# Kernel optimization log

Measured on AMD Instinct MI355X. Metric: run time of the kernel, lower is better.

## Reference

```python
import jax, jax.numpy as jnp
import numpy as np

ADJ_SIZE = 512
START_POS = 128
END_POS = 384
IN_FEATURES = 128
OUT_FEATURES = 128
BATCH = 64
BN_EPS = 1e-5


def setup_inputs() -> dict:
    key = jax.random.key(0)
    k1, k2, k3 = jax.random.split(key, 3)
    inputs = {
        "input": jax.random.normal(k1, (BATCH, ADJ_SIZE, IN_FEATURES), dtype=jnp.float32),
        "adj": jax.random.uniform(k2, (BATCH, ADJ_SIZE, ADJ_SIZE), dtype=jnp.float32),
        "weight": jax.random.normal(k3, (IN_FEATURES, OUT_FEATURES), dtype=jnp.float32) * (1.0 / np.sqrt(IN_FEATURES)),
        "gamma": jnp.ones((OUT_FEATURES * ADJ_SIZE,), dtype=jnp.float32),
        "beta": jnp.zeros((OUT_FEATURES * ADJ_SIZE,), dtype=jnp.float32),
    }
    return inputs


def _crop_mask(n, s, e, dtype):
    # zeros everywhere except the [s:e, s:e] crop block, set to 1
    idx = jnp.arange(n)
    in_crop = (idx >= s) & (idx < e)
    return (in_crop[:, None] & in_crop[None, :]).astype(dtype)  # [N, N]


def reference(input, adj, weight, gamma, beta):
    B, N, _ = input.shape
    # support = input @ weight : [B, N, F_out]
    support = jnp.einsum('bni,io->bno', input, weight)
    # mask adjacency to the crop block
    mask = _crop_mask(N, START_POS, END_POS, adj.dtype)
    adj_ = adj * mask  # [B, N, N]
    # aggregated output : [B, N, F_out]
    output_ = jnp.einsum('bnm,bmf->bnf', adj_, support)
    F = output_.shape[2]
    # BatchNorm1d over flattened (N * F) features, training-mode batch stats
    x = output_.reshape(B, N * F)
    mean = jnp.mean(x, axis=0)
    var = jnp.mean(jnp.square(x - mean), axis=0)  # biased variance (torch BN)
    x_hat = (x - mean) * jax.lax.rsqrt(var + BN_EPS)
    y = x_hat * gamma + beta
    return y.reshape(B, N, F)
```

## Files before the change

### kernel.cpp

```cpp
#include <hip/hip_runtime.h>
#include <hip/hip_bf16.h>

#define BATCH 64
#define NADJ  512
#define F     128
#define CROP0 128
#define CROP1 384
#define CN    256
#define BN_EPS 1e-5f

typedef __attribute__((ext_vector_type(8))) short short8;
typedef __attribute__((ext_vector_type(4))) float f32x4;

__device__ __forceinline__ ushort f2bf(float x) {
  __hip_bfloat16 h = __float2bfloat16(x);
  return *reinterpret_cast<ushort*>(&h);
}

__device__ __forceinline__ float bf2f(ushort u) {
  const unsigned v = (unsigned)u << 16;
  float f;
  __builtin_memcpy(&f, &v, 4);
  return f;
}

__device__ __forceinline__ short8 cvt8(const float4 a, const float4 b) {
  short8 r;
  r[0] = (short)f2bf(a.x); r[1] = (short)f2bf(a.y);
  r[2] = (short)f2bf(a.z); r[3] = (short)f2bf(a.w);
  r[4] = (short)f2bf(b.x); r[5] = (short)f2bf(b.y);
  r[6] = (short)f2bf(b.z); r[7] = (short)f2bf(b.w);
  return r;
}

__global__ __launch_bounds__(512, 1) void gcn_ka(
    const float* __restrict__ input, const float* __restrict__ adj,
    const float* __restrict__ W, const float* __restrict__ beta,
    float* __restrict__ out, ushort* __restrict__ Ocrop) {
  const int x = blockIdx.x & 7, y = blockIdx.x >> 3;
  const int b  = ((y >> 2) << 3) | x;
  const int qt = y & 3;
  __shared__ ushort wt[128][136];
  __shared__ ushort ain[2][64][136];
  __shared__ ushort stl[128][268];
  const int tid = threadIdx.x;
  const int l = tid & 63, w = tid >> 6;
  const int lr = l & 15, lg = l >> 4;

  const int n0  = qt * 64 + (w & 3) * 16;
  const int wf0 = (w >> 2) * 64;
  const float* a0 =
      adj + ((size_t)b * NADJ + CROP0 + n0 + lr) * NADJ + CROP0;
  float4 xreg[16];
#pragma unroll
  for (int ks = 0; ks < 8; ++ks) {
    const int k0 = ks * 32 + lg * 8;
    xreg[2 * ks]     = *reinterpret_cast<const float4*>(&a0[k0]);
    xreg[2 * ks + 1] = *reinterpret_cast<const float4*>(&a0[k0 + 4]);
  }

  {
    const int gid = blockIdx.x * 512 + tid;
#pragma unroll
    for (int q = 0; q < 4; ++q) {
      const int g2 = gid + q * 131072;
      const int c4 = (g2 & 31) * 4;
      const int rr = (g2 >> 5) & 255;
      const int bb = g2 >> 13;
      const int n  = rr < 128 ? rr : rr + 256;
      const float4 bv =
          *reinterpret_cast<const float4*>(&beta[(size_t)n * F + c4]);
      *reinterpret_cast<float4*>(&out[((size_t)bb * NADJ + n) * F + c4]) = bv;
    }
  }

  {
    const int i0 = tid & 63;
    const int fq = (tid >> 6) * 16;
#pragma unroll
    for (int ih = 0; ih < 2; ++ih) {
      const int i = i0 + ih * 64;
      const float* wr = &W[(size_t)i * F + fq];
      float4 v[4];
#pragma unroll
      for (int q = 0; q < 4; ++q)
        v[q] = reinterpret_cast<const float4*>(wr)[q];
#pragma unroll
      for (int q = 0; q < 4; ++q) {
        wt[fq + q * 4 + 0][i] = f2bf(v[q].x);
        wt[fq + q * 4 + 1][i] = f2bf(v[q].y);
        wt[fq + q * 4 + 2][i] = f2bf(v[q].z);
        wt[fq + q * 4 + 3][i] = f2bf(v[q].w);
      }
    }
  }

  const float* inb = input + ((size_t)b * NADJ + CROP0) * F;
  const int msub = (w & 3) * 16;
  const int sf0  = (w >> 2) * 64;
  const int ml0  = tid >> 5;
  const int ic4  = (tid & 31) * 4;
  float4 pv[4];
#pragma unroll
  for (int q = 0; q < 4; ++q)
    pv[q] = *reinterpret_cast<const float4*>(
        &inb[(size_t)(ml0 + q * 16) * F + ic4]);

  short8 areg[8];
#pragma unroll
  for (int ks = 0; ks < 8; ++ks)
    areg[ks] = cvt8(xreg[2 * ks], xreg[2 * ks + 1]);

#pragma unroll
  for (int q = 0; q < 4; ++q)
    *reinterpret_cast<ushort4*>(&ain[0][ml0 + q * 16][ic4]) =
        make_ushort4(f2bf(pv[q].x), f2bf(pv[q].y), f2bf(pv[q].z),
                     f2bf(pv[q].w));
  __syncthreads();

  f32x4 acc[4] = {};
#pragma unroll
  for (int cc = 0; cc < 4; ++cc) {
    const int mc = cc * 64;
    if (cc < 3) {
#pragma unroll
      for (int q = 0; q < 4; ++q)
        pv[q] = *reinterpret_cast<const float4*>(
            &inb[(size_t)(mc + 64 + ml0 + q * 16) * F + ic4]);
    }
    if (cc > 0) {
      const int kb0 = mc - 64;
#pragma unroll
      for (int ks2 = 0; ks2 < 2; ++ks2) {
        const int ks = (cc - 1) * 2 + ks2;
        const int k0 = kb0 + ks2 * 32 + lg * 8;
#pragma unroll
        for (int fi = 0; fi < 4; ++fi) {
          const short8 bv =
              *reinterpret_cast<const short8*>(&stl[wf0 + fi * 16 + lr][k0]);
          acc[fi] = __builtin_amdgcn_mfma_f32_16x16x32_bf16(areg[ks], bv,
                                                            acc[fi], 0, 0, 0);
        }
      }
    }
    f32x4 sacc[4] = {};
#pragma unroll
    for (int ks = 0; ks < 4; ++ks) {
      const int k0 = ks * 32 + lg * 8;
      const short8 av =
          *reinterpret_cast<const short8*>(&ain[cc & 1][msub + lr][k0]);
#pragma unroll
      for (int fi = 0; fi < 4; ++fi) {
        const short8 bv =
            *reinterpret_cast<const short8*>(&wt[sf0 + fi * 16 + lr][k0]);
        sacc[fi] =
            __builtin_amdgcn_mfma_f32_16x16x32_bf16(av, bv, sacc[fi], 0, 0, 0);
      }
    }
#pragma unroll
    for (int fi = 0; fi < 4; ++fi)
      *reinterpret_cast<ushort4*>(
          &stl[sf0 + fi * 16 + lr][mc + msub + lg * 4]) =
          make_ushort4(f2bf(sacc[fi][0]), f2bf(sacc[fi][1]),
                       f2bf(sacc[fi][2]), f2bf(sacc[fi][3]));
    if (cc < 3) {
#pragma unroll
      for (int q = 0; q < 4; ++q)
        *reinterpret_cast<ushort4*>(&ain[(cc + 1) & 1][ml0 + q * 16][ic4]) =
            make_ushort4(f2bf(pv[q].x), f2bf(pv[q].y), f2bf(pv[q].z),
                         f2bf(pv[q].w));
    }
    __syncthreads();
  }

#pragma unroll
  for (int ks2 = 0; ks2 < 2; ++ks2) {
    const int ks = 6 + ks2;
    const int k0 = 192 + ks2 * 32 + lg * 8;
#pragma unroll
    for (int fi = 0; fi < 4; ++fi) {
      const short8 bv =
          *reinterpret_cast<const short8*>(&stl[wf0 + fi * 16 + lr][k0]);
      acc[fi] = __builtin_amdgcn_mfma_f32_16x16x32_bf16(areg[ks], bv, acc[fi],
                                                        0, 0, 0);
    }
  }

#pragma unroll
  for (int fi = 0; fi < 4; ++fi) {
    const int f = wf0 + fi * 16 + lr;
    const int n = n0 + lg * 4;
#pragma unroll
    for (int r = 0; r < 4; ++r)
      Ocrop[((size_t)b * CN + n + r) * F + f] = f2bf(acc[fi][r]);
  }
}

__global__ __launch_bounds__(256) void gcn_kb(
    const ushort* __restrict__ Ocrop, float* __restrict__ out,
    const float* __restrict__ gamma, const float* __restrict__ beta) {
  __shared__ f32x4 s_l[256], s2_l[256];
  __shared__ f32x4 m_l[32], r_l[32];
  const int tid = threadIdx.x;
  const int qq = tid & 31, bg = tid >> 5;
  const int j  = (blockIdx.x * 32 + qq) * 4;
  const int nl = j >> 7, f = j & 127;
  const int nf = (CROP0 + nl) * F + f;
  const ushort* p = Ocrop + (size_t)j + (size_t)bg * 8 * CN * F;

  f32x4 x[8];
  f32x4 s = {0.f, 0.f, 0.f, 0.f}, s2 = {0.f, 0.f, 0.f, 0.f};
#pragma unroll
  for (int bb = 0; bb < 8; ++bb) {
    const ushort4 u =
        *reinterpret_cast<const ushort4*>(&p[(size_t)bb * CN * F]);
    f32x4 v;
    v[0] = bf2f(u.x); v[1] = bf2f(u.y); v[2] = bf2f(u.z); v[3] = bf2f(u.w);
    x[bb] = v;
    s += v;
    s2 += v * v;
  }
  s_l[tid]  = s;
  s2_l[tid] = s2;
  __syncthreads();
  if (tid < 32) {
    f32x4 ts = {0.f, 0.f, 0.f, 0.f}, ts2 = {0.f, 0.f, 0.f, 0.f};
#pragma unroll
    for (int g = 0; g < 8; ++g) {
      ts += s_l[g * 32 + tid];
      ts2 += s2_l[g * 32 + tid];
    }
    const f32x4 mean = ts * (1.f / BATCH);
    const f32x4 var  = ts2 * (1.f / BATCH) - mean * mean;
    f32x4 rs;
    rs[0] = rsqrtf(var[0] + BN_EPS);
    rs[1] = rsqrtf(var[1] + BN_EPS);
    rs[2] = rsqrtf(var[2] + BN_EPS);
    rs[3] = rsqrtf(var[3] + BN_EPS);
    m_l[tid] = mean;
    r_l[tid] = rs;
  }
  __syncthreads();
  const f32x4 mean = m_l[qq];
  const f32x4 rs   = r_l[qq];
  const float4 gm = *reinterpret_cast<const float4*>(&gamma[nf]);
  const float4 bt = *reinterpret_cast<const float4*>(&beta[nf]);
  f32x4 a, c;
  a[0] = rs[0] * gm.x; a[1] = rs[1] * gm.y;
  a[2] = rs[2] * gm.z; a[3] = rs[3] * gm.w;
  c[0] = bt.x - mean[0] * a[0]; c[1] = bt.y - mean[1] * a[1];
  c[2] = bt.z - mean[2] * a[2]; c[3] = bt.w - mean[3] * a[3];
#pragma unroll
  for (int bb = 0; bb < 8; ++bb) {
    const f32x4 y = x[bb] * a + c;
    *reinterpret_cast<f32x4*>(
        &out[(size_t)nf + (size_t)(bg * 8 + bb) * NADJ * F]) = y;
  }
}

extern "C" void kernel_launch(void* const* d_in, const int* in_sizes, int n_in,
                              void* d_out, int out_size, void* d_ws,
                              size_t ws_size, hipStream_t stream) {
  const float* input = (const float*)d_in[0];
  const float* adj   = (const float*)d_in[1];
  const float* W     = (const float*)d_in[2];
  const float* gamma = (const float*)d_in[3];
  const float* beta  = (const float*)d_in[4];
  float* out = (float*)d_out;

  ushort* Ocrop = (ushort*)d_ws;

  gcn_ka<<<256, 512, 0, stream>>>(input, adj, W, beta, out, Ocrop);
  gcn_kb<<<256, 256, 0, stream>>>(Ocrop, out, gamma, beta);
}
```

Measured before the change: 23.15 us.

## Reassociate GCN product as (adj·X)·W to avoid redundant support computation

Instead of each block recomputing the full support X·W for the crop and then multiplying by its adjacency rows, each block first computes adj_block·X and then multiplies that 64-row result by W. This removes the redundant per-block full-crop X·W and roughly halves the matrix-core work per block. The input is now loaded and transposed into LDS in one pass rather than double-buffered chunks, which removes overlap and adds scalar transposed LDS stores. The intermediate is rounded to bf16 at a different point, which changes numerics slightly.

```diff
diff --git a/kernel.cpp b/kernel.cpp
--- a/kernel.cpp
+++ b/kernel.cpp
@@ -40,17 +40,17 @@
   const int x = blockIdx.x & 7, y = blockIdx.x >> 3;
   const int b  = ((y >> 2) << 3) | x;
   const int qt = y & 3;
+  __shared__ ushort xt[128][280];
   __shared__ ushort wt[128][136];
-  __shared__ ushort ain[2][64][136];
-  __shared__ ushort stl[128][268];
+  __shared__ ushort tt[64][136];
   const int tid = threadIdx.x;
   const int l = tid & 63, w = tid >> 6;
   const int lr = l & 15, lg = l >> 4;
 
-  const int n0  = qt * 64 + (w & 3) * 16;
-  const int wf0 = (w >> 2) * 64;
+  const int n0w = qt * 64 + (w & 3) * 16;
+  const int wh  = w >> 2;
   const float* a0 =
-      adj + ((size_t)b * NADJ + CROP0 + n0 + lr) * NADJ + CROP0;
+      adj + ((size_t)b * NADJ + CROP0 + n0w + lr) * NADJ + CROP0;
   float4 xreg[16];
 #pragma unroll
   for (int ks = 0; ks < 8; ++ks) {
@@ -96,100 +96,69 @@
   }
 
   const float* inb = input + ((size_t)b * NADJ + CROP0) * F;
-  const int msub = (w & 3) * 16;
-  const int sf0  = (w >> 2) * 64;
-  const int ml0  = tid >> 5;
-  const int ic4  = (tid & 31) * 4;
-  float4 pv[4];
-#pragma unroll
-  for (int q = 0; q < 4; ++q)
-    pv[q] = *reinterpret_cast<const float4*>(
-        &inb[(size_t)(ml0 + q * 16) * F + ic4]);
+#pragma unroll
+  for (int q = 0; q < 16; ++q) {
+    const int idx = tid + q * 512;
+    const int m   = idx >> 5;
+    const int c4  = (idx & 31) * 4;
+    const float4 v =
+        *reinterpret_cast<const float4*>(&inb[(size_t)m * F + c4]);
+    xt[c4 + 0][m] = f2bf(v.x);
+    xt[c4 + 1][m] = f2bf(v.y);
+    xt[c4 + 2][m] = f2bf(v.z);
+    xt[c4 + 3][m] = f2bf(v.w);
+  }
 
   short8 areg[8];
 #pragma unroll
   for (int ks = 0; ks < 8; ++ks)
     areg[ks] = cvt8(xreg[2 * ks], xreg[2 * ks + 1]);
 
-#pragma unroll
-  for (int q = 0; q < 4; ++q)
-    *reinterpret_cast<ushort4*>(&ain[0][ml0 + q * 16][ic4]) =
-        make_ushort4(f2bf(pv[q].x), f2bf(pv[q].y), f2bf(pv[q].z),
-                     f2bf(pv[q].w));
-  __syncthreads();
-
-  f32x4 acc[4] = {};
-#pragma unroll
-  for (int cc = 0; cc < 4; ++cc) {
-    const int mc = cc * 64;
-    if (cc < 3) {
-#pragma unroll
-      for (int q = 0; q < 4; ++q)
-        pv[q] = *reinterpret_cast<const float4*>(
-            &inb[(size_t)(mc + 64 + ml0 + q * 16) * F + ic4]);
-    }
-    if (cc > 0) {
-      const int kb0 = mc - 64;
-#pragma unroll
-      for (int ks2 = 0; ks2 < 2; ++ks2) {
-        const int ks = (cc - 1) * 2 + ks2;
-        const int k0 = kb0 + ks2 * 32 + lg * 8;
-#pragma unroll
-        for (int fi = 0; fi < 4; ++fi) {
-          const short8 bv =
-              *reinterpret_cast<const short8*>(&stl[wf0 + fi * 16 + lr][k0]);
-          acc[fi] = __builtin_amdgcn_mfma_f32_16x16x32_bf16(areg[ks], bv,
-                                                            acc[fi], 0, 0, 0);
-        }
-      }
-    }
-    f32x4 sacc[4] = {};
-#pragma unroll
-    for (int ks = 0; ks < 4; ++ks) {
-      const int k0 = ks * 32 + lg * 8;
-      const short8 av =
-          *reinterpret_cast<const short8*>(&ain[cc & 1][msub + lr][k0]);
-#pragma unroll
-      for (int fi = 0; fi < 4; ++fi) {
-        const short8 bv =
-            *reinterpret_cast<const short8*>(&wt[sf0 + fi * 16 + lr][k0]);
-        sacc[fi] =
-            __builtin_amdgcn_mfma_f32_16x16x32_bf16(av, bv, sacc[fi], 0, 0, 0);
-      }
-    }
-#pragma unroll
-    for (int fi = 0; fi < 4; ++fi)
-      *reinterpret_cast<ushort4*>(
-          &stl[sf0 + fi * 16 + lr][mc + msub + lg * 4]) =
-          make_ushort4(f2bf(sacc[fi][0]), f2bf(sacc[fi][1]),
-                       f2bf(sacc[fi][2]), f2bf(sacc[fi][3]));
-    if (cc < 3) {
-#pragma unroll
-      for (int q = 0; q < 4; ++q)
-        *reinterpret_cast<ushort4*>(&ain[(cc + 1) & 1][ml0 + q * 16][ic4]) =
-            make_ushort4(f2bf(pv[q].x), f2bf(pv[q].y), f2bf(pv[q].z),
-                         f2bf(pv[q].w));
-    }
-    __syncthreads();
-  }
-
-#pragma unroll
-  for (int ks2 = 0; ks2 < 2; ++ks2) {
-    const int ks = 6 + ks2;
-    const int k0 = 192 + ks2 * 32 + lg * 8;
+  __syncthreads();
+
+  const int if0 = wh * 64;
+  f32x4 accT[4] = {};
+#pragma unroll
+  for (int ks = 0; ks < 8; ++ks) {
+    const int k0 = ks * 32 + lg * 8;
 #pragma unroll
     for (int fi = 0; fi < 4; ++fi) {
       const short8 bv =
-          *reinterpret_cast<const short8*>(&stl[wf0 + fi * 16 + lr][k0]);
-      acc[fi] = __builtin_amdgcn_mfma_f32_16x16x32_bf16(areg[ks], bv, acc[fi],
-                                                        0, 0, 0);
-    }
-  }
-
+          *reinterpret_cast<const short8*>(&xt[if0 + fi * 16 + lr][k0]);
+      accT[fi] = __builtin_amdgcn_mfma_f32_16x16x32_bf16(areg[ks], bv,
+                                                         accT[fi], 0, 0, 0);
+    }
+  }
+  const int nloc = (w & 3) * 16;
 #pragma unroll
   for (int fi = 0; fi < 4; ++fi) {
-    const int f = wf0 + fi * 16 + lr;
-    const int n = n0 + lg * 4;
+    const int i = if0 + fi * 16 + lr;
+#pragma unroll
+    for (int r = 0; r < 4; ++r)
+      tt[nloc + lg * 4 + r][i] = f2bf(accT[fi][r]);
+  }
+  __syncthreads();
+
+  const int f0 = wh * 64;
+  f32x4 acc[4] = {};
+#pragma unroll
+  for (int ks = 0; ks < 4; ++ks) {
+    const int k0 = ks * 32 + lg * 8;
+    const short8 av =
+        *reinterpret_cast<const short8*>(&tt[nloc + lr][k0]);
+#pragma unroll
+    for (int fi = 0; fi < 4; ++fi) {
+      const short8 bv =
+          *reinterpret_cast<const short8*>(&wt[f0 + fi * 16 + lr][k0]);
+      acc[fi] =
+          __builtin_amdgcn_mfma_f32_16x16x32_bf16(av, bv, acc[fi], 0, 0, 0);
+    }
+  }
+
+#pragma unroll
+  for (int fi = 0; fi < 4; ++fi) {
+    const int f = f0 + fi * 16 + lr;
+    const int n = n0w + lg * 4;
 #pragma unroll
     for (int r = 0; r < 4; ++r)
       Ocrop[((size_t)b * CN + n + r) * F + f] = f2bf(acc[fi][r]);
@@ -252,9 +221,9 @@
   c[2] = bt.z - mean[2] * a[2]; c[3] = bt.w - mean[3] * a[3];
 #pragma unroll
   for (int bb = 0; bb < 8; ++bb) {
-    const f32x4 y = x[bb] * a + c;
+    const f32x4 yv = x[bb] * a + c;
     *reinterpret_cast<f32x4*>(
-        &out[(size_t)nf + (size_t)(bg * 8 + bb) * NADJ * F]) = y;
+        &out[(size_t)nf + (size_t)(bg * 8 + bb) * NADJ * F]) = yv;
   }
 }
 
```

Measured after the change: 25.00 us. 8.0% more time.
